# Performance work log

Hardware: AMD Instinct MI355X
Metric: run time of the kernel (lower is better)

Reference implementation:

```python
import jax, jax.numpy as jnp
import numpy as np

NU, NI, E, C = 100000, 50000, 500000, 128
TAU = 1.0
TEMP = 0.1

def _cos(a, b):
    # torch F.cosine_similarity: dot / (max(|a|,eps) * max(|b|,eps)), eps=1e-8
    na = jnp.maximum(jnp.linalg.norm(a, axis=-1), 1e-8)
    nb = jnp.maximum(jnp.linalg.norm(b, axis=-1), 1e-8)
    return jnp.sum(a * b, axis=-1) / (na * nb)

def _ln(x, g, b):
    m = jnp.mean(x, axis=-1, keepdims=True)
    v = jnp.var(x, axis=-1, keepdims=True)
    return (x - m) * jax.lax.rsqrt(v + 1e-5) * g + b

def _gumbel_hard(logits, u, tau):
    # F.gumbel_softmax(hard=True) with straight-through estimator; u ~ U(0,1) supplied as input
    g = -jnp.log(-jnp.log(u * (1.0 - 2e-6) + 1e-6))
    y = jax.nn.softmax((logits + g) / tau, axis=-1)
    hard = jax.nn.one_hot(jnp.argmax(y, axis=-1), y.shape[-1], dtype=y.dtype)
    return jax.lax.stop_gradient(hard - y) + y

def _forward(x_user, x_item, item_pop, u_user, u_item,
             Wu_proj, bu_proj, Wi_proj, bi_proj,
             Wu_enc, bu_enc, Wu_act, bu_act,
             Wi_enc, bi_enc, Wi_fair, bi_fair,
             Wl_ui, Wr_ui, b_ui, Wl_iu, Wr_iu, b_iu,
             ln_u_g, ln_u_b, ln_i_g, ln_i_b,
             edge_ui, edge_iu, user_neg_idx, item_neg_idx):
    hu = x_user @ Wu_proj + bu_proj          # [NU, C] user_proj
    hi = x_item @ Wi_proj + bi_proj          # [NI, C] item_proj
    # FairUserNet (fair_score head output is discarded in original; omitted)
    eu = jax.nn.relu(hu @ Wu_enc + bu_enc)
    action_logits = eu @ Wu_act + bu_act     # [NU, 2]
    # FairItemNet
    ei = jax.nn.relu(hi @ Wi_enc + bi_enc)
    pop = jax.nn.sigmoid(item_pop)[:, None]
    item_logits = jnp.concatenate([ei, pop], axis=-1) @ Wi_fair + bi_fair  # [NI, 2]
    user_probs = _gumbel_hard(action_logits, u_user, TAU)[:, 0]
    item_probs = _gumbel_hard(item_logits, u_item, TAU)[:, 0]  # WeightedSAGEConv discards edge weights
    del item_probs
    # structural contrastive loss over positive edges
    src, dst = edge_ui[0], edge_ui[1]
    ue, ie = hu[src], hi[dst]                # [E, C] gathers
    pos = _cos(ue, ie)
    neg = _cos(ue, hi[item_neg_idx]) + _cos(hu[user_neg_idx], ie)
    pe = jnp.exp(pos / TEMP)
    ne = jnp.exp(neg / TEMP)
    struct_loss = -jnp.mean(jnp.log(pe / (pe + ne)))
    # 3 hetero SAGE layers (2 hidden + final); aggr='add' (sum), lin_l bias, lin_r no bias
    isrc, idst = edge_iu[0], edge_iu[1]
    for l in range(3):
        agg_i = jax.ops.segment_sum(hu[src], dst, num_segments=NI)    # user -> item
        agg_u = jax.ops.segment_sum(hi[isrc], idst, num_segments=NU)  # item -> user
        new_i = agg_i @ Wl_ui[l] + b_ui[l] + hi @ Wr_ui[l]
        new_u = agg_u @ Wl_iu[l] + b_iu[l] + hu @ Wr_iu[l]
        if l < 2:  # LayerNorm + dropout(eval=identity) only on the 2 hidden layers
            new_u = _ln(new_u, ln_u_g[l], ln_u_b[l])
            new_i = _ln(new_i, ln_i_g[l], ln_i_b[l])
        hu, hi = new_u, new_i
    return hu, hi, struct_loss, user_probs

def setup_inputs():
    key = jax.random.key(0)
    ks = iter(jax.random.split(key, 64))
    def N(shape, s=1.0):
        return jax.random.normal(next(ks), shape, jnp.float32) * s
    def U(shape):
        return jax.random.uniform(next(ks), shape, dtype=jnp.float32)
    def I(shape, hi):
        return jax.random.randint(next(ks), shape, 0, hi, dtype=jnp.int32)
    w = 0.05
    users = I((E,), NU)
    items = I((E,), NI)
    return {
        'x_user': N((NU, C)), 'x_item': N((NI, C)),
        'item_pop': N((NI,)),
        'u_user': U((NU, 2)), 'u_item': U((NI, 2)),
        'Wu_proj': N((C, C), w), 'bu_proj': N((C,), w),
        'Wi_proj': N((C, C), w), 'bi_proj': N((C,), w),
        'Wu_enc': N((C, C), w), 'bu_enc': N((C,), w),
        'Wu_act': N((C, 2), w), 'bu_act': N((2,), w),
        'Wi_enc': N((C, C), w), 'bi_enc': N((C,), w),
        'Wi_fair': N((C + 1, 2), w), 'bi_fair': N((2,), w),
        'Wl_ui': N((3, C, C), w), 'Wr_ui': N((3, C, C), w), 'b_ui': N((3, C), w),
        'Wl_iu': N((3, C, C), w), 'Wr_iu': N((3, C, C), w), 'b_iu': N((3, C), w),
        'ln_u_g': jnp.ones((2, C), jnp.float32), 'ln_u_b': jnp.zeros((2, C), jnp.float32),
        'ln_i_g': jnp.ones((2, C), jnp.float32), 'ln_i_b': jnp.zeros((2, C), jnp.float32),
        'edge_ui': jnp.stack([users, items]),
        'edge_iu': jnp.stack([items, users]),
        'sensitive_attr': I((NU,), 2),
        'user_neg_idx': I((E,), NU),
        'item_neg_idx': I((E,), NI),
    }

def reference(x_user, x_item, item_pop, u_user, u_item,
              Wu_proj, bu_proj, Wi_proj, bi_proj,
              Wu_enc, bu_enc, Wu_act, bu_act,
              Wi_enc, bi_enc, Wi_fair, bi_fair,
              Wl_ui, Wr_ui, b_ui, Wl_iu, Wr_iu, b_iu,
              ln_u_g, ln_u_b, ln_i_g, ln_i_b,
              edge_ui, edge_iu, sensitive_attr, user_neg_idx, item_neg_idx):
    del sensitive_attr  # only feeds the discarded user fair_score head / .item() side effects
    return _forward(x_user, x_item, item_pop, u_user, u_item,
                    Wu_proj, bu_proj, Wi_proj, bi_proj,
                    Wu_enc, bu_enc, Wu_act, bu_act,
                    Wi_enc, bi_enc, Wi_fair, bi_fair,
                    Wl_ui, Wr_ui, b_ui, Wl_iu, Wr_iu, b_iu,
                    ln_u_g, ln_u_b, ln_i_g, ln_i_b,
                    edge_ui, edge_iu, user_neg_idx, item_neg_idx)
```

## Files before the change

kernel.cpp:

```cpp
#include <hip/hip_runtime.h>

#define NUU 100000
#define NII 50000
#define NEDGE 500000
#define NROWS (NII + NUU)

typedef float f32x4 __attribute__((ext_vector_type(4)));
typedef short bf16x8 __attribute__((ext_vector_type(8)));

struct GemmP {
    const float* A1; const unsigned short* Wh1; const unsigned short* Wl1;
    const float* A2; const unsigned short* Wh2; const unsigned short* Wl2;
    const float* bias; const float* lg; const float* lb;
    float* out; float* nrm; int M; int mode;
};

__global__ __launch_bounds__(256, 2)
void gemm_dual(GemmP P0, GemmP P1, int gb0,
               const float* __restrict__ pw, const float* __restrict__ pb,
               const float* __restrict__ pu, float* __restrict__ pout)
{
    const bool sel = (blockIdx.x >= gb0);
    const GemmP P = sel ? P1 : P0;
    const int bi = sel ? (int)blockIdx.x - gb0 : (int)blockIdx.x;
    const int tid = threadIdx.x;
    const int l  = tid & 63;
    const int w  = tid >> 6;
    const int lm = l & 15;
    const int lk = l >> 4;
    const int rowb = bi * 256 + w * 64;

    f32x4 acc[4][8];
#pragma unroll
    for (int mt = 0; mt < 4; ++mt)
#pragma unroll
        for (int nt = 0; nt < 8; ++nt) acc[mt][nt] = (f32x4){0.f, 0.f, 0.f, 0.f};

    const int nmat = (P.A2 != nullptr) ? 2 : 1;
    for (int m = 0; m < nmat; ++m) {
        const float* A = m ? P.A2 : P.A1;
        const unsigned short* Wh = m ? P.Wh2 : P.Wh1;
        const unsigned short* Wl = m ? P.Wl2 : P.Wl1;
#pragma unroll
        for (int kt = 0; kt < 4; ++kt) {
            bf16x8 ah[4], al[4];
#pragma unroll
            for (int mt = 0; mt < 4; ++mt) {
                int row = rowb + mt * 16 + lm;
                int rowc = row < P.M ? row : P.M - 1;
                const float* ap = A + (size_t)rowc * 128 + kt * 32 + lk * 8;
                float4 f0 = *(const float4*)ap;
                float4 f1 = *(const float4*)(ap + 4);
                float a8[8] = {f0.x, f0.y, f0.z, f0.w, f1.x, f1.y, f1.z, f1.w};
                union { bf16x8 v; unsigned int u[4]; } H, L;
#pragma unroll
                for (int p = 0; p < 4; ++p) {
                    unsigned int u0 = __float_as_uint(a8[2 * p]);
                    unsigned int u1 = __float_as_uint(a8[2 * p + 1]);
                    H.u[p] = (u0 >> 16) | (u1 & 0xffff0000u);
                    float l0 = a8[2 * p]     - __uint_as_float(u0 & 0xffff0000u);
                    float l1 = a8[2 * p + 1] - __uint_as_float(u1 & 0xffff0000u);
                    L.u[p] = (__float_as_uint(l0) >> 16) | (__float_as_uint(l1) & 0xffff0000u);
                }
                ah[mt] = H.v;
                al[mt] = L.v;
            }
#pragma unroll
            for (int h = 0; h < 2; ++h) {
                bf16x8 bh[4], bl[4];
#pragma unroll
                for (int q = 0; q < 4; ++q) {
                    size_t fo = (size_t)((kt * 8 + h * 4 + q) * 64 + l) * 8;
                    bh[q] = *(const bf16x8*)(Wh + fo);
                    bl[q] = *(const bf16x8*)(Wl + fo);
                }
#pragma unroll
                for (int mt = 0; mt < 4; ++mt)
#pragma unroll
                    for (int q = 0; q < 4; ++q) {
                        int nt = h * 4 + q;
                        acc[mt][nt] = __builtin_amdgcn_mfma_f32_16x16x32_bf16(bh[q], ah[mt], acc[mt][nt], 0, 0, 0);
                        acc[mt][nt] = __builtin_amdgcn_mfma_f32_16x16x32_bf16(bl[q], ah[mt], acc[mt][nt], 0, 0, 0);
                        acc[mt][nt] = __builtin_amdgcn_mfma_f32_16x16x32_bf16(bh[q], al[mt], acc[mt][nt], 0, 0, 0);
                    }
            }
        }
    }

    f32x4 bv[8];
#pragma unroll
    for (int nt = 0; nt < 8; ++nt)
        bv[nt] = *(const f32x4*)(P.bias + nt * 16 + lk * 4);

#pragma unroll
    for (int mt = 0; mt < 4; ++mt) {
        int row = rowb + mt * 16 + lm;
        bool valid = row < P.M;
        float v[8][4];
#pragma unroll
        for (int nt = 0; nt < 8; ++nt)
#pragma unroll
            for (int i = 0; i < 4; ++i) v[nt][i] = acc[mt][nt][i] + bv[nt][i];
        if (P.mode == 1) {
#pragma unroll
            for (int nt = 0; nt < 8; ++nt)
#pragma unroll
                for (int i = 0; i < 4; ++i) v[nt][i] = fmaxf(v[nt][i], 0.f);
        } else if (P.mode == 2) {
            float s = 0.f, sq = 0.f;
#pragma unroll
            for (int nt = 0; nt < 8; ++nt)
#pragma unroll
                for (int i = 0; i < 4; ++i) { s += v[nt][i]; sq += v[nt][i] * v[nt][i]; }
            s  += __shfl_xor(s, 16, 64);  s  += __shfl_xor(s, 32, 64);
            sq += __shfl_xor(sq, 16, 64); sq += __shfl_xor(sq, 32, 64);
            float mean = s * (1.f / 128.f);
            float var  = sq * (1.f / 128.f) - mean * mean;
            float inv  = rsqrtf(var + 1e-5f);
#pragma unroll
            for (int nt = 0; nt < 8; ++nt) {
                f32x4 lg = *(const f32x4*)(P.lg + nt * 16 + lk * 4);
                f32x4 lb = *(const f32x4*)(P.lb + nt * 16 + lk * 4);
#pragma unroll
                for (int i = 0; i < 4; ++i) v[nt][i] = (v[nt][i] - mean) * inv * lg[i] + lb[i];
            }
        }
        if (pout != nullptr) {
            float q0 = 0.f, q1 = 0.f;
#pragma unroll
            for (int nt = 0; nt < 8; ++nt) {
                const float* pp = pw + (size_t)(nt * 16 + lk * 4) * 2;
                f32x4 pa = *(const f32x4*)pp;
                f32x4 pc = *(const f32x4*)(pp + 4);
                q0 += v[nt][0] * pa[0] + v[nt][1] * pa[2] + v[nt][2] * pc[0] + v[nt][3] * pc[2];
                q1 += v[nt][0] * pa[1] + v[nt][1] * pa[3] + v[nt][2] * pc[1] + v[nt][3] * pc[3];
            }
            q0 += __shfl_xor(q0, 16, 64); q0 += __shfl_xor(q0, 32, 64);
            q1 += __shfl_xor(q1, 16, 64); q1 += __shfl_xor(q1, 32, 64);
            if (lk == 0 && valid) {
                float l0 = q0 + pb[0], l1 = q1 + pb[1];
                float u0 = pu[2 * row], u1 = pu[2 * row + 1];
                float g0 = -logf(-logf(u0 * (1.f - 2e-6f) + 1e-6f));
                float g1 = -logf(-logf(u1 * (1.f - 2e-6f) + 1e-6f));
                float z0 = l0 + g0, z1 = l1 + g1;
                float mz = fmaxf(z0, z1);
                float e0 = expf(z0 - mz), e1 = expf(z1 - mz);
                float y0 = e0 / (e0 + e1);
                pout[row] = (z0 >= z1) ? ((1.f - y0) + y0) : 0.f;
            }
        }
        if (P.nrm != nullptr) {
            float sq = 0.f;
#pragma unroll
            for (int nt = 0; nt < 8; ++nt)
#pragma unroll
                for (int i = 0; i < 4; ++i) sq += v[nt][i] * v[nt][i];
            sq += __shfl_xor(sq, 16, 64); sq += __shfl_xor(sq, 32, 64);
            if (lk == 0 && valid) P.nrm[row] = fmaxf(sqrtf(sq), 1e-8f);
        }
        if (P.out != nullptr && valid) {
#pragma unroll
            for (int nt = 0; nt < 8; ++nt)
                *(float4*)(P.out + (size_t)row * 128 + nt * 16 + lk * 4) =
                    make_float4(v[nt][0], v[nt][1], v[nt][2], v[nt][3]);
        }
    }
}

struct WSrc { const float* p[7]; };
__global__ void wsplit_k(WSrc S, unsigned short* __restrict__ wout)
{
    int gid = blockIdx.x * 256 + threadIdx.x;
    if (gid >= 15 * 16384) return;
    int m = gid >> 14;
    int idx = gid & 16383;
    int k = idx >> 7, n = idx & 127;
    const float* src;
    if (m == 0) src = S.p[0];
    else if (m == 1) src = S.p[1];
    else if (m == 2) src = S.p[2];
    else if (m < 6)  src = S.p[3] + (size_t)(m - 3) * 16384;
    else if (m < 9)  src = S.p[4] + (size_t)(m - 6) * 16384;
    else if (m < 12) src = S.p[5] + (size_t)(m - 9) * 16384;
    else             src = S.p[6] + (size_t)(m - 12) * 16384;
    float wv = src[idx];
    unsigned int u = __float_as_uint(wv);
    unsigned short hi = (unsigned short)(u >> 16);
    float lof = wv - __uint_as_float(u & 0xffff0000u);
    unsigned short lo = (unsigned short)(__float_as_uint(lof) >> 16);
    int kt = k >> 5, kr = k & 31;
    int dst = ((kt * 8 + (n >> 4)) * 64 + ((kr >> 3) * 16 + (n & 15))) * 8 + (kr & 7);
    unsigned short* wm = wout + (size_t)m * 32768;
    wm[dst] = hi;
    wm[dst + 16384] = lo;
}

__global__ void loss_k(const float* __restrict__ hu, const float* __restrict__ hi,
                       const float* __restrict__ nu, const float* __restrict__ ni,
                       const int* __restrict__ src, const int* __restrict__ dst,
                       const int* __restrict__ uneg, const int* __restrict__ ineg,
                       float* __restrict__ loss, int ne)
{
    __shared__ float ls[8];
    int lane = threadIdx.x & 63;
    int half = lane >> 5;
    int l32 = lane & 31;
    int c4 = l32 * 4;
    int wib = threadIdx.x >> 6;
    int gw = (blockIdx.x * blockDim.x + threadIdx.x) >> 6;
    int nw = (gridDim.x * blockDim.x) >> 6;
    float part = 0.f;
    for (int ep = gw; ep < ne / 2; ep += nw) {
        int e = ep * 2 + half;
        int s = src[e], d = dst[e], un = uneg[e], in_ = ineg[e];
        float4 a = *(const float4*)(hu + (size_t)s * 128 + c4);
        float4 b = *(const float4*)(hi + (size_t)d * 128 + c4);
        float4 c = *(const float4*)(hi + (size_t)in_ * 128 + c4);
        float4 dd = *(const float4*)(hu + (size_t)un * 128 + c4);
        float p_sd = a.x * b.x + a.y * b.y + a.z * b.z + a.w * b.w;
        float p_sn = a.x * c.x + a.y * c.y + a.z * c.z + a.w * c.w;
        float p_nd = dd.x * b.x + dd.y * b.y + dd.z * b.z + dd.w * b.w;
#pragma unroll
        for (int m = 1; m < 32; m <<= 1) {
            p_sd += __shfl_xor(p_sd, m, 64);
            p_sn += __shfl_xor(p_sn, m, 64);
            p_nd += __shfl_xor(p_nd, m, 64);
        }
        if (l32 == 0) {
            float pos = p_sd / (nu[s] * ni[d]);
            float neg = p_sn / (nu[s] * ni[in_]) + p_nd / (nu[un] * ni[d]);
            float pe = expf(pos * 10.f);
            float nex = expf(neg * 10.f);
            part += -logf(pe / (pe + nex));
        }
    }
    if (l32 == 0) ls[wib * 2 + half] = part;
    __syncthreads();
    if (threadIdx.x == 0) {
        float t = 0.f;
#pragma unroll
        for (int j = 0; j < 8; ++j) t += ls[j];
        atomicAdd(loss, t * (1.f / 500000.f));
    }
}

__global__ void hist2_k(const int* __restrict__ ui_dst, const int* __restrict__ iu_dst,
                        int* __restrict__ deg)
{
    int e = blockIdx.x * blockDim.x + threadIdx.x;
    if (e < NEDGE) atomicAdd(&deg[ui_dst[e]], 1);
    else if (e < 2 * NEDGE) atomicAdd(&deg[NII + iu_dst[e - NEDGE]], 1);
}

__global__ void scan_part_k(const int* __restrict__ in, int* __restrict__ part, int N)
{
    __shared__ int wsum[4];
    int base = blockIdx.x * 1024 + threadIdx.x * 4;
    int s = 0;
    if (base + 3 < N) {
        int4 v = *(const int4*)(in + base);
        s = v.x + v.y + v.z + v.w;
    } else {
#pragma unroll
        for (int j = 0; j < 4; ++j) if (base + j < N) s += in[base + j];
    }
#pragma unroll
    for (int m = 1; m < 64; m <<= 1) s += __shfl_xor(s, m, 64);
    if ((threadIdx.x & 63) == 0) wsum[threadIdx.x >> 6] = s;
    __syncthreads();
    if (threadIdx.x == 0) part[blockIdx.x] = wsum[0] + wsum[1] + wsum[2] + wsum[3];
}

__global__ void scan_top_k(int* __restrict__ p, int nb)
{
    __shared__ int sm[256];
    int t = threadIdx.x;
    int v = (t < nb) ? p[t] : 0;
    sm[t] = v;
    __syncthreads();
    for (int o = 1; o < 256; o <<= 1) {
        int x = (t >= o) ? sm[t - o] : 0;
        __syncthreads();
        sm[t] += x;
        __syncthreads();
    }
    if (t < nb) p[t] = sm[t] - v;
}

__global__ void scan_final_k(const int* __restrict__ in, const int* __restrict__ part,
                             int* __restrict__ out, int N, int total)
{
    __shared__ int wtot[4];
    int tid = threadIdx.x;
    int lane = tid & 63, wid = tid >> 6;
    int base = blockIdx.x * 1024 + tid * 4;
    int v[4] = {0, 0, 0, 0};
    bool full = (base + 3 < N);
    if (full) {
        int4 q = *(const int4*)(in + base);
        v[0] = q.x; v[1] = q.y; v[2] = q.z; v[3] = q.w;
    } else {
#pragma unroll
        for (int j = 0; j < 4; ++j) if (base + j < N) v[j] = in[base + j];
    }
    int s = v[0] + v[1] + v[2] + v[3];
    int incl = s;
#pragma unroll
    for (int o = 1; o < 64; o <<= 1) {
        int n = __shfl_up(incl, o, 64);
        if (lane >= o) incl += n;
    }
    if (lane == 63) wtot[wid] = incl;
    __syncthreads();
    int woff = 0;
    for (int w2 = 0; w2 < wid; ++w2) woff += wtot[w2];
    int run = part[blockIdx.x] + woff + incl - s;
    if (full) {
        int4 o4 = make_int4(run, run + v[0], run + v[0] + v[1], run + v[0] + v[1] + v[2]);
        *(int4*)(out + base) = o4;
    } else {
#pragma unroll
        for (int j = 0; j < 4; ++j) {
            if (base + j < N) { out[base + j] = run; run += v[j]; }
        }
    }
    if (blockIdx.x == 0 && tid == 0) out[N] = total;
}

__global__ void fill2_k(const int* __restrict__ ui_dst, const int* __restrict__ ui_src,
                        const int* __restrict__ iu_dst, const int* __restrict__ iu_src,
                        const int* __restrict__ rowstart, int* __restrict__ cursor,
                        int* __restrict__ elist)
{
    int e = blockIdx.x * blockDim.x + threadIdx.x;
    if (e < NEDGE) {
        int d = ui_dst[e];
        int p = atomicAdd(&cursor[d], 1);
        elist[rowstart[d] + p] = ui_src[e];
    } else if (e < 2 * NEDGE) {
        int d = NII + iu_dst[e - NEDGE];
        int p = atomicAdd(&cursor[d], 1);
        elist[rowstart[d] + p] = iu_src[e - NEDGE];
    }
}

__global__ void agg_dual(const float* __restrict__ hu_c, const float* __restrict__ hi_c,
                         const int* __restrict__ rowstart, const int* __restrict__ elist,
                         float* __restrict__ hi_n, float* __restrict__ hu_n)
{
    int gt = blockIdx.x * blockDim.x + threadIdx.x;
    int w = gt >> 6, lane = gt & 63;
    if (w >= NROWS) return;
    const float* src;
    float* dst;
    if (w < NII) { src = hu_c; dst = hi_n + (size_t)w * 128; }
    else         { src = hi_c; dst = hu_n + (size_t)(w - NII) * 128; }
    int half = lane >> 5;
    int c4 = (lane & 31) * 4;
    int s0 = rowstart[w], s1 = rowstart[w + 1];
    float4 a = make_float4(0.f, 0.f, 0.f, 0.f);
    for (int e = s0 + half; e < s1; e += 2) {
        int s = elist[e];
        float4 v = *(const float4*)(src + (size_t)s * 128 + c4);
        a.x += v.x; a.y += v.y; a.z += v.z; a.w += v.w;
    }
    a.x += __shfl_xor(a.x, 32, 64);
    a.y += __shfl_xor(a.y, 32, 64);
    a.z += __shfl_xor(a.z, 32, 64);
    a.w += __shfl_xor(a.w, 32, 64);
    if (half == 0)
        *(float4*)(dst + c4) = a;
}

extern "C" void kernel_launch(void* const* d_in, const int* in_sizes, int n_in,
                              void* d_out, int out_size, void* d_ws, size_t ws_size,
                              hipStream_t stream)
{
    const float* x_user  = (const float*)d_in[0];
    const float* x_item  = (const float*)d_in[1];
    const float* u_user  = (const float*)d_in[3];
    const float* Wu_proj = (const float*)d_in[5];
    const float* bu_proj = (const float*)d_in[6];
    const float* Wi_proj = (const float*)d_in[7];
    const float* bi_proj = (const float*)d_in[8];
    const float* Wu_enc  = (const float*)d_in[9];
    const float* bu_enc  = (const float*)d_in[10];
    const float* Wu_act  = (const float*)d_in[11];
    const float* bu_act  = (const float*)d_in[12];
    const float* Wl_ui = (const float*)d_in[17];
    const float* Wr_ui = (const float*)d_in[18];
    const float* b_ui  = (const float*)d_in[19];
    const float* Wl_iu = (const float*)d_in[20];
    const float* Wr_iu = (const float*)d_in[21];
    const float* b_iu  = (const float*)d_in[22];
    const float* ln_u_g = (const float*)d_in[23];
    const float* ln_u_b = (const float*)d_in[24];
    const float* ln_i_g = (const float*)d_in[25];
    const float* ln_i_b = (const float*)d_in[26];
    const int* edge_ui  = (const int*)d_in[27];
    const int* edge_iu  = (const int*)d_in[28];
    const int* user_neg = (const int*)d_in[30];
    const int* item_neg = (const int*)d_in[31];

    float* out = (float*)d_out;
    float* out_hu   = out;
    float* out_hi   = out + (size_t)NUU * 128;
    float* out_loss = out + 19200000;
    float* out_prob = out + 19200001;

    float* hu0  = (float*)d_ws;
    float* hi0  = hu0 + (size_t)NUU * 128;
    float* nu   = hi0 + (size_t)NII * 128;
    float* ni   = nu + NUU;
    int* ip   = (int*)(ni + NII);
    int* rs   = ip;  ip += NROWS + 16;
    int* cur  = ip;  ip += NROWS;
    int* el   = ip;  ip += 2 * NEDGE;
    int* pt   = ip;  ip += 160;
    unsigned short* wsp = (unsigned short*)ip;

    const int* ui_src = edge_ui;
    const int* ui_dst = edge_ui + NEDGE;
    const int* iu_src = edge_iu;
    const int* iu_dst = edge_iu + NEDGE;

    const int GB_U = (NUU + 255) / 256, GB_I = (NII + 255) / 256;
    const int PB = (NROWS + 1023) / 1024;

    WSrc ws7 = {{Wu_proj, Wi_proj, Wu_enc, Wl_ui, Wr_ui, Wl_iu, Wr_iu}};
    wsplit_k<<<(15 * 16384 + 255) / 256, 256, 0, stream>>>(ws7, wsp);
    unsigned short* wm[15];
    for (int m = 0; m < 15; ++m) wm[m] = wsp + (size_t)m * 32768;

    GemmP pu_ = {x_user, wm[0], wm[0] + 16384, nullptr, nullptr, nullptr,
                 bu_proj, nullptr, nullptr, hu0, nu, NUU, 0};
    GemmP pi_ = {x_item, wm[1], wm[1] + 16384, nullptr, nullptr, nullptr,
                 bi_proj, nullptr, nullptr, hi0, ni, NII, 0};
    gemm_dual<<<GB_U + GB_I, 256, 0, stream>>>(pu_, pi_, GB_U, nullptr, nullptr, nullptr, nullptr);
    GemmP pe_ = {hu0, wm[2], wm[2] + 16384, nullptr, nullptr, nullptr,
                 bu_enc, nullptr, nullptr, nullptr, nullptr, NUU, 1};
    gemm_dual<<<GB_U, 256, 0, stream>>>(pe_, pe_, GB_U, Wu_act, bu_act, u_user, out_prob);
    hipMemsetAsync(out_loss, 0, 4, stream);
    loss_k<<<2048, 256, 0, stream>>>(hu0, hi0, nu, ni, ui_src, ui_dst, user_neg, item_neg, out_loss, NEDGE);
    hipMemsetAsync(cur, 0, (size_t)NROWS * 4, stream);
    hist2_k<<<(2 * NEDGE + 255) / 256, 256, 0, stream>>>(ui_dst, iu_dst, cur);
    scan_part_k<<<PB, 256, 0, stream>>>(cur, pt, NROWS);
    scan_top_k<<<1, 256, 0, stream>>>(pt, PB);
    scan_final_k<<<PB, 256, 0, stream>>>(cur, pt, rs, NROWS, 2 * NEDGE);
    hipMemsetAsync(cur, 0, (size_t)NROWS * 4, stream);
    fill2_k<<<(2 * NEDGE + 255) / 256, 256, 0, stream>>>(ui_dst, ui_src, iu_dst, iu_src, rs, cur, el);

    float* hu_c = hu0; float* hi_c = hi0;
    float* hu_n = out_hu; float* hi_n = out_hi;
    for (int l = 0; l < 3; ++l) {
        int mode = (l < 2) ? 2 : 0;
        agg_dual<<<NROWS / 4, 256, 0, stream>>>(hu_c, hi_c, rs, el, hi_n, hu_n);
        GemmP li_ = {hi_n, wm[3 + l], wm[3 + l] + 16384, hi_c, wm[6 + l], wm[6 + l] + 16384,
                     b_ui + l * 128, ln_i_g + (l < 2 ? l : 0) * 128, ln_i_b + (l < 2 ? l : 0) * 128,
                     hi_n, nullptr, NII, mode};
        GemmP lu_ = {hu_n, wm[9 + l], wm[9 + l] + 16384, hu_c, wm[12 + l], wm[12 + l] + 16384,
                     b_iu + l * 128, ln_u_g + (l < 2 ? l : 0) * 128, ln_u_b + (l < 2 ? l : 0) * 128,
                     hu_n, nullptr, NUU, mode};
        gemm_dual<<<GB_I + GB_U, 256, 0, stream>>>(li_, lu_, GB_I, nullptr, nullptr, nullptr, nullptr);
        float* t;
        t = hu_c; hu_c = hu_n; hu_n = t;
        t = hi_c; hi_c = hi_n; hi_n = t;
    }
}
```

Measured before the change: 994.3 us.

## Store fp16 shadow copies of node features for gather-heavy loss and aggregation

The GEMM epilogues now also write an fp16 copy of the user and item embeddings, and the contrastive-loss and neighbor-aggregation kernels gather these half-precision rows instead of fp32. Each lane handles 8 halves, so a wave covers four edges at a time. This roughly halves the bytes moved by the random gathers that dominate those kernels. The cost is an extra store in the GEMM epilogue and a loss of precision in the aggregated sums and the loss, which may go beyond the tolerance.

Result: faster. 879.3 us (-11.6%).

```diff
diff --git a/kernel.cpp b/kernel.cpp
--- a/kernel.cpp
+++ b/kernel.cpp
@@ -7,12 +7,14 @@
 
 typedef float f32x4 __attribute__((ext_vector_type(4)));
 typedef short bf16x8 __attribute__((ext_vector_type(8)));
+typedef _Float16 half8v __attribute__((ext_vector_type(8)));
+typedef _Float16 half4v __attribute__((ext_vector_type(4)));
 
 struct GemmP {
     const float* A1; const unsigned short* Wh1; const unsigned short* Wl1;
     const float* A2; const unsigned short* Wh2; const unsigned short* Wl2;
     const float* bias; const float* lg; const float* lb;
-    float* out; float* nrm; int M; int mode;
+    float* out; _Float16* out16; float* nrm; int M; int mode;
 };
 
 __global__ __launch_bounds__(256, 2)
@@ -158,11 +160,22 @@
             sq += __shfl_xor(sq, 16, 64); sq += __shfl_xor(sq, 32, 64);
             if (lk == 0 && valid) P.nrm[row] = fmaxf(sqrtf(sq), 1e-8f);
         }
-        if (P.out != nullptr && valid) {
-#pragma unroll
-            for (int nt = 0; nt < 8; ++nt)
-                *(float4*)(P.out + (size_t)row * 128 + nt * 16 + lk * 4) =
-                    make_float4(v[nt][0], v[nt][1], v[nt][2], v[nt][3]);
+        if (valid) {
+            if (P.out != nullptr) {
+#pragma unroll
+                for (int nt = 0; nt < 8; ++nt)
+                    *(float4*)(P.out + (size_t)row * 128 + nt * 16 + lk * 4) =
+                        make_float4(v[nt][0], v[nt][1], v[nt][2], v[nt][3]);
+            }
+            if (P.out16 != nullptr) {
+#pragma unroll
+                for (int nt = 0; nt < 8; ++nt) {
+                    half4v h;
+#pragma unroll
+                    for (int i = 0; i < 4; ++i) h[i] = (_Float16)v[nt][i];
+                    *(half4v*)(P.out16 + (size_t)row * 128 + nt * 16 + lk * 4) = h;
+                }
+            }
         }
     }
 }
@@ -195,38 +208,42 @@
     wm[dst + 16384] = lo;
 }
 
-__global__ void loss_k(const float* __restrict__ hu, const float* __restrict__ hi,
+__global__ void loss_k(const _Float16* __restrict__ hu16, const _Float16* __restrict__ hi16,
                        const float* __restrict__ nu, const float* __restrict__ ni,
                        const int* __restrict__ src, const int* __restrict__ dst,
                        const int* __restrict__ uneg, const int* __restrict__ ineg,
                        float* __restrict__ loss, int ne)
 {
-    __shared__ float ls[8];
+    __shared__ float ls[4];
     int lane = threadIdx.x & 63;
-    int half = lane >> 5;
-    int l32 = lane & 31;
-    int c4 = l32 * 4;
+    int q = lane >> 4;
+    int c8 = (lane & 15) * 8;
     int wib = threadIdx.x >> 6;
     int gw = (blockIdx.x * blockDim.x + threadIdx.x) >> 6;
     int nw = (gridDim.x * blockDim.x) >> 6;
     float part = 0.f;
-    for (int ep = gw; ep < ne / 2; ep += nw) {
-        int e = ep * 2 + half;
+    for (int eb = gw; eb < ne / 4; eb += nw) {
+        int e = eb * 4 + q;
         int s = src[e], d = dst[e], un = uneg[e], in_ = ineg[e];
-        float4 a = *(const float4*)(hu + (size_t)s * 128 + c4);
-        float4 b = *(const float4*)(hi + (size_t)d * 128 + c4);
-        float4 c = *(const float4*)(hi + (size_t)in_ * 128 + c4);
-        float4 dd = *(const float4*)(hu + (size_t)un * 128 + c4);
-        float p_sd = a.x * b.x + a.y * b.y + a.z * b.z + a.w * b.w;
-        float p_sn = a.x * c.x + a.y * c.y + a.z * c.z + a.w * c.w;
-        float p_nd = dd.x * b.x + dd.y * b.y + dd.z * b.z + dd.w * b.w;
-#pragma unroll
-        for (int m = 1; m < 32; m <<= 1) {
+        half8v a = *(const half8v*)(hu16 + (size_t)s * 128 + c8);
+        half8v b = *(const half8v*)(hi16 + (size_t)d * 128 + c8);
+        half8v c = *(const half8v*)(hi16 + (size_t)in_ * 128 + c8);
+        half8v dd = *(const half8v*)(hu16 + (size_t)un * 128 + c8);
+        float p_sd = 0.f, p_sn = 0.f, p_nd = 0.f;
+#pragma unroll
+        for (int j = 0; j < 8; ++j) {
+            float af = (float)a[j], bf = (float)b[j];
+            p_sd += af * bf;
+            p_sn += af * (float)c[j];
+            p_nd += (float)dd[j] * bf;
+        }
+#pragma unroll
+        for (int m = 1; m < 16; m <<= 1) {
             p_sd += __shfl_xor(p_sd, m, 64);
             p_sn += __shfl_xor(p_sn, m, 64);
             p_nd += __shfl_xor(p_nd, m, 64);
         }
-        if (l32 == 0) {
+        if ((lane & 15) == 0) {
             float pos = p_sd / (nu[s] * ni[d]);
             float neg = p_sn / (nu[s] * ni[in_]) + p_nd / (nu[un] * ni[d]);
             float pe = expf(pos * 10.f);
@@ -234,14 +251,12 @@
             part += -logf(pe / (pe + nex));
         }
     }
-    if (l32 == 0) ls[wib * 2 + half] = part;
+    part += __shfl_xor(part, 16, 64);
+    part += __shfl_xor(part, 32, 64);
+    if (lane == 0) ls[wib] = part;
     __syncthreads();
-    if (threadIdx.x == 0) {
-        float t = 0.f;
-#pragma unroll
-        for (int j = 0; j < 8; ++j) t += ls[j];
-        atomicAdd(loss, t * (1.f / 500000.f));
-    }
+    if (threadIdx.x == 0)
+        atomicAdd(loss, (ls[0] + ls[1] + ls[2] + ls[3]) * (1.f / 500000.f));
 }
 
 __global__ void hist2_k(const int* __restrict__ ui_dst, const int* __restrict__ iu_dst,
@@ -344,32 +359,36 @@
     }
 }
 
-__global__ void agg_dual(const float* __restrict__ hu_c, const float* __restrict__ hi_c,
+__global__ void agg_dual(const _Float16* __restrict__ hu16, const _Float16* __restrict__ hi16,
                          const int* __restrict__ rowstart, const int* __restrict__ elist,
                          float* __restrict__ hi_n, float* __restrict__ hu_n)
 {
     int gt = blockIdx.x * blockDim.x + threadIdx.x;
     int w = gt >> 6, lane = gt & 63;
     if (w >= NROWS) return;
-    const float* src;
+    const _Float16* src;
     float* dst;
-    if (w < NII) { src = hu_c; dst = hi_n + (size_t)w * 128; }
-    else         { src = hi_c; dst = hu_n + (size_t)(w - NII) * 128; }
-    int half = lane >> 5;
-    int c4 = (lane & 31) * 4;
+    if (w < NII) { src = hu16; dst = hi_n + (size_t)w * 128; }
+    else         { src = hi16; dst = hu_n + (size_t)(w - NII) * 128; }
+    int q = lane >> 4;
+    int c8 = (lane & 15) * 8;
     int s0 = rowstart[w], s1 = rowstart[w + 1];
-    float4 a = make_float4(0.f, 0.f, 0.f, 0.f);
-    for (int e = s0 + half; e < s1; e += 2) {
+    float a[8] = {0.f, 0.f, 0.f, 0.f, 0.f, 0.f, 0.f, 0.f};
+    for (int e = s0 + q; e < s1; e += 4) {
         int s = elist[e];
-        float4 v = *(const float4*)(src + (size_t)s * 128 + c4);
-        a.x += v.x; a.y += v.y; a.z += v.z; a.w += v.w;
-    }
-    a.x += __shfl_xor(a.x, 32, 64);
-    a.y += __shfl_xor(a.y, 32, 64);
-    a.z += __shfl_xor(a.z, 32, 64);
-    a.w += __shfl_xor(a.w, 32, 64);
-    if (half == 0)
-        *(float4*)(dst + c4) = a;
+        half8v v = *(const half8v*)(src + (size_t)s * 128 + c8);
+#pragma unroll
+        for (int j = 0; j < 8; ++j) a[j] += (float)v[j];
+    }
+#pragma unroll
+    for (int j = 0; j < 8; ++j) {
+        a[j] += __shfl_xor(a[j], 16, 64);
+        a[j] += __shfl_xor(a[j], 32, 64);
+    }
+    if (lane < 16) {
+        *(float4*)(dst + c8)     = make_float4(a[0], a[1], a[2], a[3]);
+        *(float4*)(dst + c8 + 4) = make_float4(a[4], a[5], a[6], a[7]);
+    }
 }
 
 extern "C" void kernel_launch(void* const* d_in, const int* in_sizes, int n_in,
@@ -418,6 +437,8 @@
     int* el   = ip;  ip += 2 * NEDGE;
     int* pt   = ip;  ip += 160;
     unsigned short* wsp = (unsigned short*)ip;
+    _Float16* hu16 = (_Float16*)(wsp + 15 * 32768);
+    _Float16* hi16 = hu16 + (size_t)NUU * 128;
 
     const int* ui_src = edge_ui;
     const int* ui_dst = edge_ui + NEDGE;
@@ -433,15 +454,15 @@
     for (int m = 0; m < 15; ++m) wm[m] = wsp + (size_t)m * 32768;
 
     GemmP pu_ = {x_user, wm[0], wm[0] + 16384, nullptr, nullptr, nullptr,
-                 bu_proj, nullptr, nullptr, hu0, nu, NUU, 0};
+                 bu_proj, nullptr, nullptr, hu0, hu16, nu, NUU, 0};
     GemmP pi_ = {x_item, wm[1], wm[1] + 16384, nullptr, nullptr, nullptr,
-                 bi_proj, nullptr, nullptr, hi0, ni, NII, 0};
+                 bi_proj, nullptr, nullptr, hi0, hi16, ni, NII, 0};
     gemm_dual<<<GB_U + GB_I, 256, 0, stream>>>(pu_, pi_, GB_U, nullptr, nullptr, nullptr, nullptr);
     GemmP pe_ = {hu0, wm[2], wm[2] + 16384, nullptr, nullptr, nullptr,
-                 bu_enc, nullptr, nullptr, nullptr, nullptr, NUU, 1};
+                 bu_enc, nullptr, nullptr, nullptr, nullptr, nullptr, NUU, 1};
     gemm_dual<<<GB_U, 256, 0, stream>>>(pe_, pe_, GB_U, Wu_act, bu_act, u_user, out_prob);
     hipMemsetAsync(out_loss, 0, 4, stream);
-    loss_k<<<2048, 256, 0, stream>>>(hu0, hi0, nu, ni, ui_src, ui_dst, user_neg, item_neg, out_loss, NEDGE);
+    loss_k<<<2048, 256, 0, stream>>>(hu16, hi16, nu, ni, ui_src, ui_dst, user_neg, item_neg, out_loss, NEDGE);
     hipMemsetAsync(cur, 0, (size_t)NROWS * 4, stream);
     hist2_k<<<(2 * NEDGE + 255) / 256, 256, 0, stream>>>(ui_dst, iu_dst, cur);
     scan_part_k<<<PB, 256, 0, stream>>>(cur, pt, NROWS);
@@ -454,13 +475,13 @@
     float* hu_n = out_hu; float* hi_n = out_hi;
     for (int l = 0; l < 3; ++l) {
         int mode = (l < 2) ? 2 : 0;
-        agg_dual<<<NROWS / 4, 256, 0, stream>>>(hu_c, hi_c, rs, el, hi_n, hu_n);
+        agg_dual<<<NROWS / 4, 256, 0, stream>>>(hu16, hi16, rs, el, hi_n, hu_n);
         GemmP li_ = {hi_n, wm[3 + l], wm[3 + l] + 16384, hi_c, wm[6 + l], wm[6 + l] + 16384,
                      b_ui + l * 128, ln_i_g + (l < 2 ? l : 0) * 128, ln_i_b + (l < 2 ? l : 0) * 128,
-                     hi_n, nullptr, NII, mode};
+                     hi_n, (l < 2) ? hi16 : nullptr, nullptr, NII, mode};
         GemmP lu_ = {hu_n, wm[9 + l], wm[9 + l] + 16384, hu_c, wm[12 + l], wm[12 + l] + 16384,
                      b_iu + l * 128, ln_u_g + (l < 2 ? l : 0) * 128, ln_u_b + (l < 2 ? l : 0) * 128,
-                     hu_n, nullptr, NUU, mode};
+                     hu_n, (l < 2) ? hu16 : nullptr, nullptr, NUU, mode};
         gemm_dual<<<GB_I + GB_U, 256, 0, stream>>>(li_, lu_, GB_I, nullptr, nullptr, nullptr, nullptr);
         float* t;
         t = hu_c; hu_c = hu_n; hu_n = t;
```
